# Kernel tuning notes

Measured on AMD Instinct MI355X. Metric: run time of the kernel, lower is better.

Reference implementation:

```python
import jax, jax.numpy as jnp
import numpy as np

B, N, D = 1, 2048, 1024
L, H, DH = 4, 16, 64
INNER = H * DH            # 1024, == D
FF = int(D * 4.0)         # 4096 (GEGLU inner)
SCALE = DH ** -0.5
LN_EPS = 1e-5


def setup_inputs() -> dict:
    key = jax.random.key(0)
    ks = jax.random.split(key, 8)
    w = 0.02
    inp = {
        'x': jax.random.normal(ks[0], (B, N, D), jnp.float32),
        'mask': jnp.ones((B, N), dtype=bool),
        # stacked per-layer params (leading dim L)
        'Wqkv': jax.random.normal(ks[1], (L, D, 3 * INNER), jnp.float32) * w,
        'Wo': jax.random.normal(ks[2], (L, INNER, D), jnp.float32) * w,
        'bo': jnp.zeros((L, D), jnp.float32),
        'ln1_g': jnp.ones((L, D), jnp.float32),
        'ln1_b': jnp.zeros((L, D), jnp.float32),
        'ln2_g': jnp.ones((L, D), jnp.float32),
        'ln2_b': jnp.zeros((L, D), jnp.float32),
        'ls1': jnp.full((L, D), 0.1, jnp.float32),  # LayerScale init_eps=0.1 (depth<=18)
        'ls2': jnp.full((L, D), 0.1, jnp.float32),
        'W1': jax.random.normal(ks[3], (L, D, 2 * FF), jnp.float32) * w,
        'b1': jnp.zeros((L, 2 * FF), jnp.float32),
        'W2': jax.random.normal(ks[4], (L, FF, D), jnp.float32) * w,
        'b2': jnp.zeros((L, D), jnp.float32),
    }
    return inp


def _layernorm(x, g, b):
    mu = jnp.mean(x, axis=-1, keepdims=True)
    var = jnp.mean(jnp.square(x - mu), axis=-1, keepdims=True)
    return (x - mu) * jax.lax.rsqrt(var + LN_EPS) * g + b


def _forward(x, mask, Wqkv, Wo, bo, ln1_g, ln1_b, ln2_g, ln2_b, ls1, ls2, W1, b1, W2, b2):
    n = x.shape[1]
    causal = jnp.arange(n)[None, :] > jnp.arange(n)[:, None]  # True = masked
    valid = mask[:, None, None, :] & ~causal[None, None]       # (B,1,N,N) True = keep
    for l in range(L):
        # --- attention sublayer: x + LayerScale(PreNorm(Attn))(x) ---
        h = _layernorm(x, ln1_g[l], ln1_b[l])
        qkv = h @ Wqkv[l]                                      # (B,N,3*INNER)
        q, k, v = jnp.split(qkv, 3, axis=-1)
        q = q.reshape(B, n, H, DH).transpose(0, 2, 1, 3) * SCALE
        k = k.reshape(B, n, H, DH).transpose(0, 2, 1, 3)
        v = v.reshape(B, n, H, DH).transpose(0, 2, 1, 3)
        dots = jnp.einsum('bhid,bhjd->bhij', q, k)             # (B,H,N,N)
        neg = -jnp.finfo(dots.dtype).max
        dots = jnp.where(valid, dots, neg)
        attn = jax.nn.softmax(dots, axis=-1)                   # stable_softmax, temp=1
        o = jnp.einsum('bhij,bhjd->bhid', attn, v)
        o = o.transpose(0, 2, 1, 3).reshape(B, n, INNER)
        o = o @ Wo[l] + bo[l]
        x = x + o * ls1[l]
        # --- feedforward sublayer: x + LayerScale(PreNorm(GEGLU-FFN))(x) ---
        h = _layernorm(x, ln2_g[l], ln2_b[l])
        u = h @ W1[l] + b1[l]                                  # (B,N,2*FF)
        a, g = jnp.split(u, 2, axis=-1)
        f = (a * jax.nn.gelu(g, approximate=False)) @ W2[l] + b2[l]
        x = x + f * ls2[l]
    return x


def reference(x, mask, Wqkv, Wo, bo, ln1_g, ln1_b, ln2_g, ln2_b, ls1, ls2, W1, b1, W2, b2):
    return _forward(x, mask, Wqkv, Wo, bo, ln1_g, ln1_b, ln2_g, ln2_b, ls1, ls2, W1, b1, W2, b2)
```

## Files before the change

kernel.cpp:

```cpp
#include <hip/hip_runtime.h>
#include <hip/hip_bf16.h>
#include <math.h>

#define LN_EPS 1e-5f
#define ATT_SCALE 0.125f

typedef __bf16 bf16x8 __attribute__((ext_vector_type(8)));
typedef float f32x4 __attribute__((ext_vector_type(4)));

__device__ __forceinline__ unsigned short f2bf(float f){
  unsigned int u = __builtin_bit_cast(unsigned int, f);
  u += 0x7fffu + ((u >> 16) & 1u);
  return (unsigned short)(u >> 16);
}
__device__ __forceinline__ float bfbits2f(unsigned int lo16){
  return __builtin_bit_cast(float, lo16 << 16);
}

__global__ __launch_bounds__(256) void ln_kernel(
    const float* __restrict__ X, const float* __restrict__ g,
    const float* __restrict__ b, unsigned short* __restrict__ H)
{
  __shared__ float red[4];
  int row = blockIdx.x, t = threadIdx.x;
  const float4 xv = ((const float4*)(X + (size_t)row*1024))[t];
  float s = xv.x + xv.y + xv.z + xv.w;
  #pragma unroll
  for (int o=32;o;o>>=1) s += __shfl_down(s,o);
  if ((t&63)==0) red[t>>6] = s;
  __syncthreads();
  float mu = (red[0]+red[1]+red[2]+red[3]) * (1.f/1024.f);
  __syncthreads();
  float dx = xv.x-mu, dy = xv.y-mu, dz = xv.z-mu, dw = xv.w-mu;
  float s2 = dx*dx+dy*dy+dz*dz+dw*dw;
  #pragma unroll
  for (int o=32;o;o>>=1) s2 += __shfl_down(s2,o);
  if ((t&63)==0) red[t>>6] = s2;
  __syncthreads();
  float var = (red[0]+red[1]+red[2]+red[3]) * (1.f/1024.f);
  float rs = rsqrtf(var + LN_EPS);
  const float4 gv = ((const float4*)g)[t];
  const float4 bv = ((const float4*)b)[t];
  ushort4 o4;
  o4.x = f2bf(dx*rs*gv.x + bv.x);
  o4.y = f2bf(dy*rs*gv.y + bv.y);
  o4.z = f2bf(dz*rs*gv.z + bv.z);
  o4.w = f2bf(dw*rs*gv.w + bv.w);
  ((ushort4*)(H + (size_t)row*1024))[t] = o4;
}

template<int SK, int DO_LN>
__global__ __launch_bounds__(256) void redln_kernel(
    const float* __restrict__ P, float* __restrict__ X,
    const float* __restrict__ bias, const float* __restrict__ scale,
    const float* __restrict__ g, const float* __restrict__ b,
    unsigned short* __restrict__ H)
{
  __shared__ float red[4];
  int row = blockIdx.x, t = threadIdx.x;
  size_t off = (size_t)row*1024 + t*4;
  float4 xv = *(const float4*)(X + off);
  float4 pv = *(const float4*)(P + off);
  #pragma unroll
  for (int c=1;c<SK;c++){
    float4 q = *(const float4*)(P + (size_t)c*2048*1024 + off);
    pv.x+=q.x; pv.y+=q.y; pv.z+=q.z; pv.w+=q.w;
  }
  const float4 bv = ((const float4*)bias)[t];
  const float4 sv = ((const float4*)scale)[t];
  xv.x += (pv.x+bv.x)*sv.x;
  xv.y += (pv.y+bv.y)*sv.y;
  xv.z += (pv.z+bv.z)*sv.z;
  xv.w += (pv.w+bv.w)*sv.w;
  *(float4*)(X + off) = xv;
  if (DO_LN){
    float s = xv.x + xv.y + xv.z + xv.w;
    #pragma unroll
    for (int o=32;o;o>>=1) s += __shfl_down(s,o);
    if ((t&63)==0) red[t>>6] = s;
    __syncthreads();
    float mu = (red[0]+red[1]+red[2]+red[3]) * (1.f/1024.f);
    __syncthreads();
    float dx = xv.x-mu, dy = xv.y-mu, dz = xv.z-mu, dw = xv.w-mu;
    float s2 = dx*dx+dy*dy+dz*dz+dw*dw;
    #pragma unroll
    for (int o=32;o;o>>=1) s2 += __shfl_down(s2,o);
    if ((t&63)==0) red[t>>6] = s2;
    __syncthreads();
    float var = (red[0]+red[1]+red[2]+red[3]) * (1.f/1024.f);
    float rs = rsqrtf(var + LN_EPS);
    const float4 gv = ((const float4*)g)[t];
    const float4 lbv = ((const float4*)b)[t];
    ushort4 o4;
    o4.x = f2bf(dx*rs*gv.x + lbv.x);
    o4.y = f2bf(dy*rs*gv.y + lbv.y);
    o4.z = f2bf(dz*rs*gv.z + lbv.z);
    o4.w = f2bf(dw*rs*gv.w + lbv.w);
    ((ushort4*)(H + (size_t)row*1024))[t] = o4;
  }
}

__global__ __launch_bounds__(256) void trc_kernel(
    const float* __restrict__ W, unsigned short* __restrict__ WT, int K, int N)
{
  __shared__ float tile[64][65];
  int n0 = blockIdx.x*64, k0 = blockIdx.y*64;
  int t = threadIdx.x;
  int tx = t & 63, ty = t >> 6;
  #pragma unroll
  for (int p=0;p<16;p++){
    int r = ty*16+p;
    tile[r][tx] = W[(size_t)(k0+r)*N + n0 + tx];
  }
  __syncthreads();
  int kc = t & 31, tb = t >> 5;
  #pragma unroll
  for (int p=0;p<8;p++){
    int nr = tb + p*8;
    unsigned int lo = f2bf(tile[2*kc][nr]);
    unsigned int hi = f2bf(tile[2*kc+1][nr]);
    ((unsigned int*)(WT + (size_t)(n0+nr)*K + k0))[kc] = lo | (hi<<16);
  }
}

__global__ __launch_bounds__(256) void trc_w1_kernel(
    const float* __restrict__ W, unsigned short* __restrict__ WT)
{
  __shared__ float tile[64][65];
  int n0 = blockIdx.x*64, k0 = blockIdx.y*64;
  int ca = (n0>>5)*16;
  int t = threadIdx.x;
  int tx = t & 63, ty = t >> 6;
  #pragma unroll
  for (int p=0;p<16;p++){
    int r = ty*16+p;
    int col = (tx < 32) ? (ca + tx) : (ca + 4064 + tx);
    tile[r][tx] = W[(size_t)(k0+r)*8192 + col];
  }
  __syncthreads();
  int kc = t & 31, tb = t >> 5;
  #pragma unroll
  for (int p=0;p<8;p++){
    int nr = tb + p*8;
    int rr = nr & 31;
    int vcol = (nr>>5)*16 + (rr&15) + ((rr>>4)<<5);
    unsigned int lo = f2bf(tile[2*kc][vcol]);
    unsigned int hi = f2bf(tile[2*kc+1][vcol]);
    ((unsigned int*)(WT + (size_t)(n0+nr)*1024 + k0))[kc] = lo | (hi<<16);
  }
}

template<int MODE>
__global__ __launch_bounds__(256) void gemm_bt(
    const unsigned short* __restrict__ A, const unsigned short* __restrict__ BT,
    int M, int N, int K,
    float* __restrict__ Xres, unsigned short* __restrict__ Obf,
    const float* __restrict__ bias, const float* __restrict__ scale)
{
  __shared__ unsigned short Asm[128*64];
  __shared__ unsigned short Bsm[128*64];
  int t = threadIdx.x;
  int lane = t & 63;
  int w = t >> 6, wm = w >> 1, wn = w & 1;

  int nwg = gridDim.x * gridDim.y;
  int wg = blockIdx.y * gridDim.x + blockIdx.x;
  int cpx = nwg >> 3;
  int swz = (wg & 7) * cpx + (wg >> 3);
  int bn = swz % gridDim.x, bm = swz / gridDim.x;

  f32x4 acc[4][4] = {};
  int ktBeg = 0, ktEnd = K >> 6;
  if (MODE == 3){
    int per = (K >> 6) / gridDim.z;
    ktBeg = blockIdx.z * per;
    ktEnd = ktBeg + per;
  }

  for (int kt = ktBeg; kt < ktEnd; ++kt){
    #pragma unroll
    for (int c=0;c<4;c++){
      int li = c*256 + t;
      int row = li >> 3, sc = li & 7;
      int gc = sc ^ (row & 7);
      const unsigned short* sa = A  + (size_t)(bm*128 + row)*K + kt*64 + gc*8;
      const unsigned short* sb = BT + (size_t)(bn*128 + row)*K + kt*64 + gc*8;
      __builtin_amdgcn_global_load_lds(
        (const __attribute__((address_space(1))) unsigned int*)sa,
        (__attribute__((address_space(3))) unsigned int*)(Asm + (size_t)(c*256 + (t & ~63))*8),
        16, 0, 0);
      __builtin_amdgcn_global_load_lds(
        (const __attribute__((address_space(1))) unsigned int*)sb,
        (__attribute__((address_space(3))) unsigned int*)(Bsm + (size_t)(c*256 + (t & ~63))*8),
        16, 0, 0);
    }
    __syncthreads();
    #pragma unroll
    for (int kk=0;kk<2;kk++){
      bf16x8 aF[4], bF[4];
      #pragma unroll
      for (int m=0;m<4;m++){
        int row = wm*64 + m*16 + (lane&15);
        int ch = kk*4 + (lane>>4);
        aF[m] = *(const bf16x8*)&Asm[row*64 + (ch ^ (row&7))*8];
      }
      #pragma unroll
      for (int n=0;n<4;n++){
        int row = wn*64 + n*16 + (lane&15);
        int ch = kk*4 + (lane>>4);
        bF[n] = *(const bf16x8*)&Bsm[row*64 + (ch ^ (row&7))*8];
      }
      #pragma unroll
      for (int m=0;m<4;m++)
        #pragma unroll
        for (int n=0;n<4;n++)
          acc[m][n] = __builtin_amdgcn_mfma_f32_16x16x32_bf16(aF[m], bF[n], acc[m][n], 0,0,0);
    }
    __syncthreads();
  }

  int colg = lane & 15;
  if (MODE==4){
    float b1a[2], b1g[2];
    #pragma unroll
    for (int p=0;p<2;p++){
      int oc = (bn*4 + wn*2 + p)*16 + colg;
      b1a[p] = bias[oc];
      b1g[p] = bias[oc + 4096];
    }
    #pragma unroll
    for (int m=0;m<4;m++){
      int gr0 = bm*128 + wm*64 + m*16 + (lane>>4)*4;
      #pragma unroll
      for (int p=0;p<2;p++){
        int ocol = (bn*4 + wn*2 + p)*16 + colg;
        #pragma unroll
        for (int j=0;j<4;j++){
          float va = acc[m][2*p][j]   + b1a[p];
          float vg = acc[m][2*p+1][j] + b1g[p];
          float f = va * (0.5f * vg * (1.f + erff(vg * 0.70710678118f)));
          Obf[(size_t)(gr0+j)*4096 + ocol] = f2bf(f);
        }
      }
    }
    return;
  }
  #pragma unroll
  for (int m=0;m<4;m++){
    int gr0 = bm*128 + wm*64 + m*16 + (lane>>4)*4;
    #pragma unroll
    for (int n=0;n<4;n++){
      int gc = bn*128 + wn*64 + n*16 + colg;
      #pragma unroll
      for (int j=0;j<4;j++){
        int gr = gr0 + j;
        float v = acc[m][n][j];
        if (MODE==0){
          Obf[(size_t)gr*N + gc] = f2bf(v);
        } else {
          Xres[(size_t)blockIdx.z*((size_t)M*N) + (size_t)gr*N + gc] = v;
        }
      }
    }
  }
}

__global__ __launch_bounds__(256) void vtr_kernel(
    const unsigned short* __restrict__ qkv, unsigned short* __restrict__ VT)
{
  __shared__ unsigned int tile[64][33];
  int h = blockIdx.y;
  int n0 = blockIdx.x * 64;
  int t = threadIdx.x;
  #pragma unroll
  for (int p=0;p<8;p++){
    int idx = p*256 + t;
    int r = idx >> 5, c = idx & 31;
    tile[r][c] = *(const unsigned int*)(qkv + (size_t)(n0+r)*3072 + 2048 + h*64 + c*2);
  }
  __syncthreads();
  #pragma unroll
  for (int p=0;p<8;p++){
    int idx = p*256 + t;
    int d = idx >> 5, c = idx & 31;
    unsigned int a = tile[2*c][d>>1];
    unsigned int b = tile[2*c+1][d>>1];
    unsigned int lo = (d&1) ? (a>>16) : (a & 0xffffu);
    unsigned int hi = (d&1) ? (b>>16) : (b & 0xffffu);
    *(unsigned int*)(VT + (size_t)h*131072 + (size_t)d*2048 + n0 + c*2) = lo | (hi<<16);
  }
}

__global__ __launch_bounds__(256) void flash_attn(
    const unsigned short* __restrict__ qkv,
    const unsigned short* __restrict__ VT,
    unsigned short* __restrict__ O)
{
  __shared__ unsigned short Klds[64*64];
  __shared__ unsigned short Vlds[64*64];
  __shared__ unsigned short Plds[4][16*72];
  __shared__ float fbuf[4][16];
  __shared__ float lbuf[4][16];

  int t = threadIdx.x;
  int lane = t & 63;
  int w = t >> 6;
  int q15 = lane & 15, l16 = lane >> 4;

  int bid = blockIdx.x;
  int half = bid >> 8, idx = bid & 255;
  int h = (idx >> 5) + half*8;
  int qt = half ? (31 - (idx & 31)) : (idx & 31);
  int q0 = qt * 64;

  bf16x8 qF[2];
  int qrow = q0 + w*16 + q15;
  #pragma unroll
  for (int db=0; db<2; db++)
    qF[db] = *(const bf16x8*)(qkv + (size_t)qrow*3072 + h*64 + db*32 + l16*8);

  f32x4 o[4] = {};
  float m_run = -1e30f, l_run = 0.f;

  for (int kt = 0; kt <= qt; ++kt){
    int k0 = kt*64;
    #pragma unroll
    for (int c=0;c<2;c++){
      int li = c*256 + t;
      int row = li >> 3, sc = li & 7;
      int gc = sc ^ (row & 7);
      const unsigned short* sk = qkv + (size_t)(k0+row)*3072 + 1024 + h*64 + gc*8;
      const unsigned short* sv = VT + (size_t)h*131072 + (size_t)row*2048 + k0 + gc*8;
      __builtin_amdgcn_global_load_lds(
        (const __attribute__((address_space(1))) unsigned int*)sk,
        (__attribute__((address_space(3))) unsigned int*)(Klds + (c*256 + (t & ~63))*8),
        16, 0, 0);
      __builtin_amdgcn_global_load_lds(
        (const __attribute__((address_space(1))) unsigned int*)sv,
        (__attribute__((address_space(3))) unsigned int*)(Vlds + (c*256 + (t & ~63))*8),
        16, 0, 0);
    }
    __syncthreads();

    f32x4 s[4] = {};
    #pragma unroll
    for (int km=0;km<4;km++){
      #pragma unroll
      for (int db=0;db<2;db++){
        int row = km*16 + q15;
        int ch = db*4 + l16;
        bf16x8 kF = *(const bf16x8*)&Klds[row*64 + (ch ^ (row&7))*8];
        s[km] = __builtin_amdgcn_mfma_f32_16x16x32_bf16(kF, qF[db], s[km], 0,0,0);
      }
    }

    bool diag = (kt == qt);
    float pmax = -1e30f;
    #pragma unroll
    for (int km=0;km<4;km++){
      #pragma unroll
      for (int j=0;j<4;j++){
        float sv = s[km][j] * ATT_SCALE;
        if (diag){
          int kg = km*16 + l16*4 + j;
          int qg = w*16 + q15;
          if (kg > qg) sv = -1e30f;
        }
        s[km][j] = sv;
        pmax = fmaxf(pmax, sv);
      }
    }
    pmax = fmaxf(pmax, __shfl_xor(pmax, 16));
    pmax = fmaxf(pmax, __shfl_xor(pmax, 32));

    float m_new = fmaxf(m_run, pmax);
    float f = __expf(m_run - m_new);

    float lsum = 0.f;
    #pragma unroll
    for (int km=0;km<4;km++){
      float p0 = __expf(s[km][0]-m_new);
      float p1 = __expf(s[km][1]-m_new);
      float p2 = __expf(s[km][2]-m_new);
      float p3 = __expf(s[km][3]-m_new);
      lsum += (p0+p1)+(p2+p3);
      unsigned int u0 = (unsigned int)f2bf(p0) | ((unsigned int)f2bf(p1)<<16);
      unsigned int u1 = (unsigned int)f2bf(p2) | ((unsigned int)f2bf(p3)<<16);
      *(uint2*)&Plds[w][q15*72 + km*16 + l16*4] = make_uint2(u0,u1);
    }
    lsum += __shfl_xor(lsum,16);
    lsum += __shfl_xor(lsum,32);
    l_run = l_run * f + lsum;
    m_run = m_new;

    if (l16 == 0) fbuf[w][q15] = f;
    f32x4 fv = *(f32x4*)&fbuf[w][l16*4];
    #pragma unroll
    for (int n=0;n<4;n++) o[n] *= fv;

    #pragma unroll
    for (int kb=0;kb<2;kb++){
      bf16x8 aP = *(const bf16x8*)&Plds[w][q15*72 + kb*32 + l16*8];
      #pragma unroll
      for (int n=0;n<4;n++){
        int row = n*16 + q15;
        int ch = kb*4 + l16;
        bf16x8 vF = *(const bf16x8*)&Vlds[row*64 + (ch ^ (row&7))*8];
        o[n] = __builtin_amdgcn_mfma_f32_16x16x32_bf16(aP, vF, o[n], 0,0,0);
      }
    }
    __syncthreads();
  }

  if (l16 == 0) lbuf[w][q15] = 1.f / l_run;
  f32x4 lv = *(f32x4*)&lbuf[w][l16*4];

  #pragma unroll
  for (int n=0;n<4;n++){
    #pragma unroll
    for (int j=0;j<4;j++){
      int row = q0 + w*16 + l16*4 + j;
      int col = h*64 + n*16 + q15;
      O[(size_t)row*1024 + col] = f2bf(o[n][j]*lv[j]);
    }
  }
}

extern "C" void kernel_launch(void* const* d_in, const int* in_sizes, int n_in,
                              void* d_out, int out_size, void* d_ws, size_t ws_size,
                              hipStream_t stream)
{
  (void)in_sizes; (void)n_in; (void)out_size; (void)ws_size;
  const float* x_in = (const float*)d_in[0];
  const float* Wqkv = (const float*)d_in[2];
  const float* Wo   = (const float*)d_in[3];
  const float* bo   = (const float*)d_in[4];
  const float* ln1g = (const float*)d_in[5];
  const float* ln1b = (const float*)d_in[6];
  const float* ln2g = (const float*)d_in[7];
  const float* ln2b = (const float*)d_in[8];
  const float* ls1  = (const float*)d_in[9];
  const float* ls2  = (const float*)d_in[10];
  const float* W1   = (const float*)d_in[11];
  const float* b1   = (const float*)d_in[12];
  const float* W2   = (const float*)d_in[13];
  const float* b2   = (const float*)d_in[14];
  float* X = (float*)d_out;

  char* ws = (char*)d_ws;
  unsigned short* WT  = (unsigned short*)(ws);
  unsigned short* hb  = (unsigned short*)(ws + (16u<<20));
  unsigned short* qu  = (unsigned short*)(ws + (20u<<20));
  unsigned short* VTg = (unsigned short*)(ws + (36u<<20));
  unsigned short* of  = (unsigned short*)(ws + (52u<<20));
  float* PT  = (float*)(ws + (20u<<20));

  hipMemcpyAsync(d_out, (const void*)x_in, (size_t)2048*1024*4,
                 hipMemcpyDeviceToDevice, stream);

  for (int l = 0; l < 4; ++l){
    if (l == 0)
      ln_kernel<<<2048,256,0,stream>>>(X, ln1g, ln1b, hb);
    trc_kernel<<<dim3(3072/64,1024/64),256,0,stream>>>(Wqkv + (size_t)l*1024*3072, WT, 1024, 3072);
    gemm_bt<0><<<dim3(3072/128,2048/128),256,0,stream>>>(hb, WT, 2048,3072,1024,
        nullptr, qu, nullptr, nullptr);
    vtr_kernel<<<dim3(32,16),256,0,stream>>>(qu, VTg);
    flash_attn<<<512,256,0,stream>>>(qu, VTg, of);
    trc_kernel<<<dim3(1024/64,1024/64),256,0,stream>>>(Wo + (size_t)l*1024*1024, WT, 1024, 1024);
    gemm_bt<3><<<dim3(1024/128,2048/128,2),256,0,stream>>>(of, WT, 2048,1024,1024,
        PT, nullptr, nullptr, nullptr);
    redln_kernel<2,1><<<2048,256,0,stream>>>(PT, X, bo + l*1024, ls1 + l*1024,
        ln2g + l*1024, ln2b + l*1024, hb);
    trc_w1_kernel<<<dim3(8192/64,1024/64),256,0,stream>>>(W1 + (size_t)l*1024*8192, WT);
    gemm_bt<4><<<dim3(8192/128,2048/128),256,0,stream>>>(hb, WT, 2048,8192,1024,
        nullptr, of, b1 + (size_t)l*8192, nullptr);
    trc_kernel<<<dim3(1024/64,4096/64),256,0,stream>>>(W2 + (size_t)l*4096*1024, WT, 4096, 1024);
    gemm_bt<3><<<dim3(1024/128,2048/128,4),256,0,stream>>>(of, WT, 2048,1024,4096,
        PT, nullptr, nullptr, nullptr);
    if (l < 3)
      redln_kernel<4,1><<<2048,256,0,stream>>>(PT, X, b2 + l*1024, ls2 + l*1024,
          ln1g + (l+1)*1024, ln1b + (l+1)*1024, hb);
    else
      redln_kernel<4,0><<<2048,256,0,stream>>>(PT, X, b2 + l*1024, ls2 + l*1024,
          nullptr, nullptr, nullptr);
  }
}
```

Measured before the change: 914.1 us.

## Double-buffer LDS tiles in GEMM and flash attention to overlap loads with MFMA

Both the GEMM and the flash-attention kernels now keep two LDS buffers and prefetch the next K tile with global_load_lds while MFMAs run on the current one. This is meant to hide global-memory latency behind compute instead of stalling at a barrier every iteration. The GEMM also raises wave priority around its MFMA block. The cost is double the LDS footprint (64KB for the GEMM), which can lower occupancy, and correctness depends on the single trailing barrier being enough, since the async loads are not explicitly waited on before the next read.

New measurement: 830.0 us. -9.2%, faster.

```diff
diff --git a/kernel.cpp b/kernel.cpp
--- a/kernel.cpp
+++ b/kernel.cpp
@@ -157,8 +157,8 @@
     float* __restrict__ Xres, unsigned short* __restrict__ Obf,
     const float* __restrict__ bias, const float* __restrict__ scale)
 {
-  __shared__ unsigned short Asm[128*64];
-  __shared__ unsigned short Bsm[128*64];
+  __shared__ unsigned short Asm[2][128*64];
+  __shared__ unsigned short Bsm[2][128*64];
   int t = threadIdx.x;
   int lane = t & 63;
   int w = t >> 6, wm = w >> 1, wn = w & 1;
@@ -177,24 +177,30 @@
     ktEnd = ktBeg + per;
   }
 
-  for (int kt = ktBeg; kt < ktEnd; ++kt){
+  int srow = t >> 3, ssc = t & 7;
+  auto STAGE = [&](int kt, int buf){
     #pragma unroll
     for (int c=0;c<4;c++){
-      int li = c*256 + t;
-      int row = li >> 3, sc = li & 7;
-      int gc = sc ^ (row & 7);
+      int row = c*32 + srow;
+      int gc = ssc ^ (row & 7);
       const unsigned short* sa = A  + (size_t)(bm*128 + row)*K + kt*64 + gc*8;
       const unsigned short* sb = BT + (size_t)(bn*128 + row)*K + kt*64 + gc*8;
       __builtin_amdgcn_global_load_lds(
         (const __attribute__((address_space(1))) unsigned int*)sa,
-        (__attribute__((address_space(3))) unsigned int*)(Asm + (size_t)(c*256 + (t & ~63))*8),
+        (__attribute__((address_space(3))) unsigned int*)(&Asm[buf][(c*256 + (t & ~63))*8]),
         16, 0, 0);
       __builtin_amdgcn_global_load_lds(
         (const __attribute__((address_space(1))) unsigned int*)sb,
-        (__attribute__((address_space(3))) unsigned int*)(Bsm + (size_t)(c*256 + (t & ~63))*8),
+        (__attribute__((address_space(3))) unsigned int*)(&Bsm[buf][(c*256 + (t & ~63))*8]),
         16, 0, 0);
     }
-    __syncthreads();
+  };
+
+  STAGE(ktBeg, 0);
+  __syncthreads();
+  int cur = 0;
+  for (int kt = ktBeg; kt < ktEnd; ++kt){
+    if (kt + 1 < ktEnd) STAGE(kt + 1, cur ^ 1);
     #pragma unroll
     for (int kk=0;kk<2;kk++){
       bf16x8 aF[4], bF[4];
@@ -202,21 +208,24 @@
       for (int m=0;m<4;m++){
         int row = wm*64 + m*16 + (lane&15);
         int ch = kk*4 + (lane>>4);
-        aF[m] = *(const bf16x8*)&Asm[row*64 + (ch ^ (row&7))*8];
+        aF[m] = *(const bf16x8*)&Asm[cur][row*64 + (ch ^ (row&7))*8];
       }
       #pragma unroll
       for (int n=0;n<4;n++){
         int row = wn*64 + n*16 + (lane&15);
         int ch = kk*4 + (lane>>4);
-        bF[n] = *(const bf16x8*)&Bsm[row*64 + (ch ^ (row&7))*8];
-      }
+        bF[n] = *(const bf16x8*)&Bsm[cur][row*64 + (ch ^ (row&7))*8];
+      }
+      __builtin_amdgcn_s_setprio(1);
       #pragma unroll
       for (int m=0;m<4;m++)
         #pragma unroll
         for (int n=0;n<4;n++)
           acc[m][n] = __builtin_amdgcn_mfma_f32_16x16x32_bf16(aF[m], bF[n], acc[m][n], 0,0,0);
+      __builtin_amdgcn_s_setprio(0);
     }
     __syncthreads();
+    cur ^= 1;
   }
 
   int colg = lane & 15;
@@ -296,8 +305,8 @@
     const unsigned short* __restrict__ VT,
     unsigned short* __restrict__ O)
 {
-  __shared__ unsigned short Klds[64*64];
-  __shared__ unsigned short Vlds[64*64];
+  __shared__ unsigned short Klds[2][64*64];
+  __shared__ unsigned short Vlds[2][64*64];
   __shared__ unsigned short Plds[4][16*72];
   __shared__ float fbuf[4][16];
   __shared__ float lbuf[4][16];
@@ -319,28 +328,34 @@
   for (int db=0; db<2; db++)
     qF[db] = *(const bf16x8*)(qkv + (size_t)qrow*3072 + h*64 + db*32 + l16*8);
 
-  f32x4 o[4] = {};
-  float m_run = -1e30f, l_run = 0.f;
-
-  for (int kt = 0; kt <= qt; ++kt){
+  int srow = t >> 3, ssc = t & 7;
+  auto STAGE = [&](int kt, int buf){
     int k0 = kt*64;
     #pragma unroll
     for (int c=0;c<2;c++){
-      int li = c*256 + t;
-      int row = li >> 3, sc = li & 7;
-      int gc = sc ^ (row & 7);
+      int row = c*32 + srow;
+      int gc = ssc ^ (row & 7);
       const unsigned short* sk = qkv + (size_t)(k0+row)*3072 + 1024 + h*64 + gc*8;
       const unsigned short* sv = VT + (size_t)h*131072 + (size_t)row*2048 + k0 + gc*8;
       __builtin_amdgcn_global_load_lds(
         (const __attribute__((address_space(1))) unsigned int*)sk,
-        (__attribute__((address_space(3))) unsigned int*)(Klds + (c*256 + (t & ~63))*8),
+        (__attribute__((address_space(3))) unsigned int*)(&Klds[buf][(c*256 + (t & ~63))*8]),
         16, 0, 0);
       __builtin_amdgcn_global_load_lds(
         (const __attribute__((address_space(1))) unsigned int*)sv,
-        (__attribute__((address_space(3))) unsigned int*)(Vlds + (c*256 + (t & ~63))*8),
+        (__attribute__((address_space(3))) unsigned int*)(&Vlds[buf][(c*256 + (t & ~63))*8]),
         16, 0, 0);
     }
-    __syncthreads();
+  };
+
+  f32x4 o[4] = {};
+  float m_run = -1e30f, l_run = 0.f;
+
+  STAGE(0, 0);
+  __syncthreads();
+  int cur = 0;
+  for (int kt = 0; kt <= qt; ++kt){
+    if (kt < qt) STAGE(kt + 1, cur ^ 1);
 
     f32x4 s[4] = {};
     #pragma unroll
@@ -349,7 +364,7 @@
       for (int db=0;db<2;db++){
         int row = km*16 + q15;
         int ch = db*4 + l16;
-        bf16x8 kF = *(const bf16x8*)&Klds[row*64 + (ch ^ (row&7))*8];
+        bf16x8 kF = *(const bf16x8*)&Klds[cur][row*64 + (ch ^ (row&7))*8];
         s[km] = __builtin_amdgcn_mfma_f32_16x16x32_bf16(kF, qF[db], s[km], 0,0,0);
       }
     }
@@ -405,11 +420,12 @@
       for (int n=0;n<4;n++){
         int row = n*16 + q15;
         int ch = kb*4 + l16;
-        bf16x8 vF = *(const bf16x8*)&Vlds[row*64 + (ch ^ (row&7))*8];
+        bf16x8 vF = *(const bf16x8*)&Vlds[cur][row*64 + (ch ^ (row&7))*8];
         o[n] = __builtin_amdgcn_mfma_f32_16x16x32_bf16(aP, vF, o[n], 0,0,0);
       }
     }
     __syncthreads();
+    cur ^= 1;
   }
 
   if (l16 == 0) lbuf[w][q15] = 1.f / l_run;
```
